# Kernel optimization log

Hardware: AMD Instinct MI355X
Metric: run time of the kernel (lower is better)

## Reference

```python
import jax, jax.numpy as jnp
import numpy as np

B, T, C, HS = 4, 4096, 1024, 64


def setup_inputs() -> dict:
    key = jax.random.key(0)
    kx, kq, kk, kv = jax.random.split(key, 4)
    x = jax.random.normal(kx, (B, T, C), dtype=jnp.float32)
    s = 1.0 / np.sqrt(C)
    Wq = jax.random.normal(kq, (C, HS), dtype=jnp.float32) * s
    Wk = jax.random.normal(kk, (C, HS), dtype=jnp.float32) * s
    Wv = jax.random.normal(kv, (C, HS), dtype=jnp.float32) * s
    return {"x": x, "Wq": Wq, "Wk": Wk, "Wv": Wv}


def reference(x, Wq, Wk, Wv):
    # q,k,v: [B, T, HS]
    q = x @ Wq
    k = x @ Wk
    v = x @ Wv
    scale = k.shape[-1] ** -0.5
    # full T x T causal attention scores, as the torch module materializes
    scores = jnp.einsum('bqh,bkh->bqk', q, k) * scale  # [B, T, T]
    t = x.shape[1]
    causal = jnp.tril(jnp.ones((t, t), dtype=bool))
    scores = jnp.where(causal[None, :, :], scores, -jnp.inf)
    wei = jax.nn.softmax(scores, axis=-1)  # dropout = 0.0 (eval)
    out = jnp.einsum('bqk,bkh->bqh', wei, v)  # [B, T, HS]
    return out
```

## Files before the change

### kernel.cpp

```cpp
#include <hip/hip_runtime.h>
#include <math.h>

#define BB 4
#define TT 4096
#define CC 1024
#define HS 64
#define MM (BB*TT)

typedef __attribute__((ext_vector_type(8))) short short8;
typedef __attribute__((ext_vector_type(4))) float f32x4;
typedef __attribute__((ext_vector_type(4))) unsigned short ushort4v;

__device__ __forceinline__ unsigned short f2bf(float f) {
    union { float f; unsigned u; } v; v.f = f;
    return (unsigned short)((v.u + 0x7fffu + ((v.u >> 16) & 1u)) >> 16);
}

__global__ __launch_bounds__(256) void prep_kernel(
    const float* __restrict__ Wq, const float* __restrict__ Wk,
    const float* __restrict__ Wv, unsigned short* __restrict__ Wt)
{
    const int which = blockIdx.x >> 4;
    const int k0 = (blockIdx.x & 15) * 64;
    const float* __restrict__ W = (which == 0) ? Wq : (which == 1) ? Wk : Wv;
    const float scale = (which == 0) ? 0.125f : 1.0f;
    __shared__ unsigned short lds[64][65];
    const int t = threadIdx.x;
    #pragma unroll
    for (int i = 0; i < 16; i++) {
        int idx = t + 256 * i;
        int r = idx >> 6, n = idx & 63;
        lds[r][n] = f2bf(W[(size_t)(k0 + r) * 64 + n] * scale);
    }
    __syncthreads();
    #pragma unroll
    for (int i = 0; i < 16; i++) {
        int idx = t + 256 * i;
        int n = idx >> 6, r = idx & 63;
        Wt[(which << 16) + (n << 10) + k0 + r] = lds[r][n];
    }
}

__global__ __launch_bounds__(256, 2) void qkv_mfma(
    const float* __restrict__ x, const unsigned short* __restrict__ Wt,
    unsigned short* __restrict__ qb, unsigned short* __restrict__ kb,
    unsigned short* __restrict__ vT)
{
    const int rt = blockIdx.x;
    __shared__ unsigned short xs[32][136];
    __shared__ unsigned short ws[192][136];

    const int t = threadIdx.x;
    const int w = t >> 6;
    const int lane = t & 63;
    const int quad = lane >> 4;
    const int c = lane & 15;

    float4 xreg[4];
    short8 wreg[12];
    #pragma unroll
    for (int i = 0; i < 4; i++) {
        int idx = t + 256 * i;
        int r = idx >> 5, c4 = (idx & 31) * 4;
        xreg[i] = *(const float4*)(x + (size_t)(rt * 32 + r) * CC + c4);
    }
    #pragma unroll
    for (int i = 0; i < 12; i++) {
        int idx = t + 256 * i;
        int n = idx >> 4, c8 = (idx & 15) * 8;
        wreg[i] = *(const short8*)(Wt + (size_t)n * CC + c8);
    }

    f32x4 acc[2][3];
    #pragma unroll
    for (int mt = 0; mt < 2; mt++)
        #pragma unroll
        for (int j = 0; j < 3; j++) acc[mt][j] = (f32x4){0.f, 0.f, 0.f, 0.f};

    for (int k0 = 0; k0 < CC; k0 += 128) {
        __syncthreads();
        #pragma unroll
        for (int i = 0; i < 4; i++) {
            int idx = t + 256 * i;
            int r = idx >> 5, c4 = (idx & 31) * 4;
            ushort4v p = { f2bf(xreg[i].x), f2bf(xreg[i].y), f2bf(xreg[i].z), f2bf(xreg[i].w) };
            *(ushort4v*)&xs[r][c4] = p;
        }
        #pragma unroll
        for (int i = 0; i < 12; i++) {
            int idx = t + 256 * i;
            int n = idx >> 4, c8 = (idx & 15) * 8;
            *(short8*)&ws[n][c8] = wreg[i];
        }
        if (k0 + 128 < CC) {
            #pragma unroll
            for (int i = 0; i < 4; i++) {
                int idx = t + 256 * i;
                int r = idx >> 5, c4 = (idx & 31) * 4;
                xreg[i] = *(const float4*)(x + (size_t)(rt * 32 + r) * CC + k0 + 128 + c4);
            }
            #pragma unroll
            for (int i = 0; i < 12; i++) {
                int idx = t + 256 * i;
                int n = idx >> 4, c8 = (idx & 15) * 8;
                wreg[i] = *(const short8*)(Wt + (size_t)n * CC + k0 + 128 + c8);
            }
        }
        __syncthreads();
        #pragma unroll
        for (int ks = 0; ks < 4; ks++) {
            short8 af[2], bf[3];
            #pragma unroll
            for (int mt = 0; mt < 2; mt++)
                af[mt] = *(const short8*)&xs[16 * mt + c][ks * 32 + quad * 8];
            #pragma unroll
            for (int j = 0; j < 3; j++)
                bf[j] = *(const short8*)&ws[16 * (w + 4 * j) + c][ks * 32 + quad * 8];
            #pragma unroll
            for (int mt = 0; mt < 2; mt++)
                #pragma unroll
                for (int j = 0; j < 3; j++)
                    acc[mt][j] = __builtin_amdgcn_mfma_f32_16x16x32_bf16(af[mt], bf[j], acc[mt][j], 0, 0, 0);
        }
    }

    __syncthreads();
    unsigned short (*vtb)[72] = (unsigned short (*)[72])ws;
    #pragma unroll
    for (int mt = 0; mt < 2; mt++) {
        int grow = rt * 32 + 16 * mt + quad * 4;
        #pragma unroll
        for (int reg = 0; reg < 4; reg++) {
            qb[(size_t)(grow + reg) * HS + 16 * w + c] = f2bf(acc[mt][0][reg]);
            kb[(size_t)(grow + reg) * HS + 16 * w + c] = f2bf(acc[mt][1][reg]);
            vtb[16 * w + c][16 * mt + quad * 4 + reg] = f2bf(acc[mt][2][reg]);
        }
    }
    __syncthreads();
    {
        const int b  = rt >> 7;
        const int t0 = (rt & 127) * 32;
        int d = t >> 2, c8 = (t & 3) * 8;
        short8 v0 = *(const short8*)&vtb[d][c8];
        *(short8*)(vT + (size_t)b * HS * TT + (size_t)d * TT + t0 + c8) = v0;
    }
}

__global__ __launch_bounds__(256, 4) void attn_mfma(
    const unsigned short* __restrict__ qb, const unsigned short* __restrict__ kb,
    const unsigned short* __restrict__ vT, float* __restrict__ Opart,
    float* __restrict__ lpart)
{
    const int bid = blockIdx.x;
    const int qt = (TT / 64 - 1) - (bid >> 4);
    const int j  = (bid >> 2) & 3;
    const int b  = bid & 3;

    __shared__ unsigned short ks[64][72];
    __shared__ unsigned short vt[64][72];
    __shared__ unsigned short ps[4][16][72];

    const int t = threadIdx.x;
    const int w = t >> 6;
    const int lane = t & 63;
    const int quad = lane >> 4;
    const int c = lane & 15;
    const int qrow = qt * 64 + 16 * w;

    short8 aq[2];
    #pragma unroll
    for (int kstep = 0; kstep < 2; kstep++)
        aq[kstep] = *(const short8*)(qb + (size_t)(b * TT + qrow + c) * HS + kstep * 32 + quad * 8);

    const int nkt = (qt >= j) ? ((qt - j) >> 2) + 1 : 0;
    const unsigned short* Kb = kb + (size_t)b * TT * HS;
    const unsigned short* Vb = vT + (size_t)b * HS * TT;

    const int srow = t >> 3;
    const int sc8  = (t & 7) * 8;

    short8 kreg[2], vreg[2];
    if (nkt > 0) {
        const int kt0 = j * 64;
        #pragma unroll
        for (int i = 0; i < 2; i++) {
            kreg[i] = *(const short8*)(Kb + (size_t)(kt0 + srow + 32 * i) * HS + sc8);
            vreg[i] = *(const short8*)(Vb + (size_t)(srow + 32 * i) * TT + kt0 + sc8);
        }
    }

    float l[4] = {0.f, 0.f, 0.f, 0.f};
    f32x4 oacc[4];
    #pragma unroll
    for (int dt = 0; dt < 4; dt++) oacc[dt] = (f32x4){0.f, 0.f, 0.f, 0.f};

    for (int i = 0; i < nkt; i++) {
        const int kt = j + 4 * i;
        const int kt0 = kt * 64;
        __syncthreads();
        #pragma unroll
        for (int ii = 0; ii < 2; ii++) {
            *(short8*)&ks[srow + 32 * ii][sc8] = kreg[ii];
            *(short8*)&vt[srow + 32 * ii][sc8] = vreg[ii];
        }
        if (i + 1 < nkt) {
            const int nb = kt0 + 256;
            #pragma unroll
            for (int ii = 0; ii < 2; ii++) {
                kreg[ii] = *(const short8*)(Kb + (size_t)(nb + srow + 32 * ii) * HS + sc8);
                vreg[ii] = *(const short8*)(Vb + (size_t)(srow + 32 * ii) * TT + nb + sc8);
            }
        }
        __syncthreads();

        f32x4 sc[4];
        #pragma unroll
        for (int st = 0; st < 4; st++) sc[st] = (f32x4){0.f, 0.f, 0.f, 0.f};
        #pragma unroll
        for (int kstep = 0; kstep < 2; kstep++) {
            #pragma unroll
            for (int st = 0; st < 4; st++) {
                short8 bf = *(const short8*)&ks[16 * st + c][kstep * 32 + quad * 8];
                sc[st] = __builtin_amdgcn_mfma_f32_16x16x32_bf16(aq[kstep], bf, sc[st], 0, 0, 0);
            }
        }
        if (kt == qt) {
            #pragma unroll
            for (int st = 0; st < 4; st++)
                #pragma unroll
                for (int reg = 0; reg < 4; reg++) {
                    int kg = kt0 + 16 * st + c;
                    int qg = qrow + quad * 4 + reg;
                    float p = (kg <= qg) ? __expf(sc[st][reg]) : 0.f;
                    sc[st][reg] = p;
                    l[reg] += p;
                }
        } else {
            #pragma unroll
            for (int st = 0; st < 4; st++)
                #pragma unroll
                for (int reg = 0; reg < 4; reg++) {
                    float p = __expf(sc[st][reg]);
                    sc[st][reg] = p;
                    l[reg] += p;
                }
        }
        #pragma unroll
        for (int st = 0; st < 4; st++)
            #pragma unroll
            for (int reg = 0; reg < 4; reg++)
                ps[w][quad * 4 + reg][16 * st + c] = f2bf(sc[st][reg]);

        #pragma unroll
        for (int kstep = 0; kstep < 2; kstep++) {
            short8 ap = *(const short8*)&ps[w][c][kstep * 32 + quad * 8];
            #pragma unroll
            for (int dt = 0; dt < 4; dt++) {
                short8 bv = *(const short8*)&vt[16 * dt + c][kstep * 32 + quad * 8];
                oacc[dt] = __builtin_amdgcn_mfma_f32_16x16x32_bf16(ap, bv, oacc[dt], 0, 0, 0);
            }
        }
    }

    #pragma unroll
    for (int reg = 0; reg < 4; reg++)
        #pragma unroll
        for (int msk = 1; msk < 16; msk <<= 1)
            l[reg] += __shfl_xor(l[reg], msk);

    float* __restrict__ Oj = Opart + (size_t)j * MM * HS;
    #pragma unroll
    for (int dt = 0; dt < 4; dt++)
        #pragma unroll
        for (int reg = 0; reg < 4; reg++)
            Oj[(size_t)(b * TT + qrow + quad * 4 + reg) * HS + 16 * dt + c] = oacc[dt][reg];
    if (c == 0)
        #pragma unroll
        for (int reg = 0; reg < 4; reg++)
            lpart[(size_t)j * MM + b * TT + qrow + quad * 4 + reg] = l[reg];
}

__global__ __launch_bounds__(256) void combine_kernel(
    const float* __restrict__ Opart, const float* __restrict__ lpart,
    float* __restrict__ out)
{
    const int id = blockIdx.x * 256 + threadIdx.x;
    const int row = id >> 4;
    float l = lpart[row] + lpart[MM + row] + lpart[2 * MM + row] + lpart[3 * MM + row];
    const float4* O = (const float4*)Opart;
    const size_t stride = (size_t)MM * HS / 4;
    float4 a = O[id], b = O[id + stride], c = O[id + 2 * stride], d = O[id + 3 * stride];
    float inv = 1.f / l;
    float4 r;
    r.x = (a.x + b.x + c.x + d.x) * inv;
    r.y = (a.y + b.y + c.y + d.y) * inv;
    r.z = (a.z + b.z + c.z + d.z) * inv;
    r.w = (a.w + b.w + c.w + d.w) * inv;
    ((float4*)out)[id] = r;
}

extern "C" void kernel_launch(void* const* d_in, const int* in_sizes, int n_in,
                              void* d_out, int out_size, void* d_ws, size_t ws_size,
                              hipStream_t stream) {
    const float* x  = (const float*)d_in[0];
    const float* Wq = (const float*)d_in[1];
    const float* Wk = (const float*)d_in[2];
    const float* Wv = (const float*)d_in[3];
    float* out = (float*)d_out;

    unsigned short* Wt   = (unsigned short*)d_ws;
    unsigned short* qbuf = Wt + 3 * 64 * 1024;
    unsigned short* kbuf = qbuf + (size_t)MM * HS;
    unsigned short* vTb  = kbuf + (size_t)MM * HS;
    float* Opart = (float*)(vTb + (size_t)MM * HS);
    float* lpart = Opart + 4 * (size_t)MM * HS;

    prep_kernel<<<48, 256, 0, stream>>>(Wq, Wk, Wv, Wt);
    qkv_mfma<<<MM / 32, 256, 0, stream>>>(x, Wt, qbuf, kbuf, vTb);
    attn_mfma<<<BB * (TT / 64) * 4, 256, 0, stream>>>(qbuf, kbuf, vTb, Opart, lpart);
    combine_kernel<<<1024, 256, 0, stream>>>(Opart, lpart, out);
}
```

Baseline: 136.8 us.

## Use 128-row query tiles with 8-way KV split and packed bf16 conversion

```diff
diff --git a/kernel.cpp b/kernel.cpp
--- a/kernel.cpp
+++ b/kernel.cpp
@@ -6,6 +6,7 @@
 #define CC 1024
 #define HS 64
 #define MM (BB*TT)
+#define KSPLIT 8
 
 typedef __attribute__((ext_vector_type(8))) short short8;
 typedef __attribute__((ext_vector_type(4))) float f32x4;
@@ -14,6 +15,12 @@
 __device__ __forceinline__ unsigned short f2bf(float f) {
     union { float f; unsigned u; } v; v.f = f;
     return (unsigned short)((v.u + 0x7fffu + ((v.u >> 16) & 1u)) >> 16);
+}
+
+__device__ __forceinline__ unsigned cvt_pk_bf16(float lo, float hi) {
+    unsigned r;
+    asm("v_cvt_pk_bf16_f32 %0, %1, %2" : "=v"(r) : "v"(lo), "v"(hi));
+    return r;
 }
 
 __global__ __launch_bounds__(256) void prep_kernel(
@@ -152,27 +159,30 @@
     float* __restrict__ lpart)
 {
     const int bid = blockIdx.x;
-    const int qt = (TT / 64 - 1) - (bid >> 4);
-    const int j  = (bid >> 2) & 3;
+    const int qt = (TT / 128 - 1) - (bid >> 5);
+    const int j  = (bid >> 2) & 7;
     const int b  = bid & 3;
 
     __shared__ unsigned short ks[64][72];
     __shared__ unsigned short vt[64][72];
-    __shared__ unsigned short ps[4][16][72];
+    __shared__ unsigned short ps[4][32][72];
 
     const int t = threadIdx.x;
     const int w = t >> 6;
     const int lane = t & 63;
     const int quad = lane >> 4;
     const int c = lane & 15;
-    const int qrow = qt * 64 + 16 * w;
-
-    short8 aq[2];
-    #pragma unroll
-    for (int kstep = 0; kstep < 2; kstep++)
-        aq[kstep] = *(const short8*)(qb + (size_t)(b * TT + qrow + c) * HS + kstep * 32 + quad * 8);
-
-    const int nkt = (qt >= j) ? ((qt - j) >> 2) + 1 : 0;
+    const int qrow = qt * 128 + 32 * w;
+
+    short8 aq[2][2];
+    #pragma unroll
+    for (int mt = 0; mt < 2; mt++)
+        #pragma unroll
+        for (int kstep = 0; kstep < 2; kstep++)
+            aq[mt][kstep] = *(const short8*)(qb + (size_t)(b * TT + qrow + 16 * mt + c) * HS + kstep * 32 + quad * 8);
+
+    const int lastkt = 2 * qt + 1;
+    const int nkt = (lastkt >= j) ? ((lastkt - j) >> 3) + 1 : 0;
     const unsigned short* Kb = kb + (size_t)b * TT * HS;
     const unsigned short* Vb = vT + (size_t)b * HS * TT;
 
@@ -189,13 +199,45 @@
         }
     }
 
-    float l[4] = {0.f, 0.f, 0.f, 0.f};
-    f32x4 oacc[4];
-    #pragma unroll
-    for (int dt = 0; dt < 4; dt++) oacc[dt] = (f32x4){0.f, 0.f, 0.f, 0.f};
+    float l[2][4] = {{0.f,0.f,0.f,0.f},{0.f,0.f,0.f,0.f}};
+    f32x4 oacc[2][4];
+    #pragma unroll
+    for (int mt = 0; mt < 2; mt++)
+        #pragma unroll
+        for (int dt = 0; dt < 4; dt++) oacc[mt][dt] = (f32x4){0.f, 0.f, 0.f, 0.f};
+
+#define SCORE_ST(MASKC) do { \
+    _Pragma("unroll") \
+    for (int st = 0; st < 4; st++) { \
+        f32x4 s[2]; \
+        s[0] = (f32x4){0.f,0.f,0.f,0.f}; s[1] = (f32x4){0.f,0.f,0.f,0.f}; \
+        _Pragma("unroll") \
+        for (int kstep = 0; kstep < 2; kstep++) { \
+            short8 bf = *(const short8*)&ks[16 * st + c][kstep * 32 + quad * 8]; \
+            s[0] = __builtin_amdgcn_mfma_f32_16x16x32_bf16(aq[0][kstep], bf, s[0], 0, 0, 0); \
+            s[1] = __builtin_amdgcn_mfma_f32_16x16x32_bf16(aq[1][kstep], bf, s[1], 0, 0, 0); \
+        } \
+        _Pragma("unroll") \
+        for (int mt = 0; mt < 2; mt++) { \
+            _Pragma("unroll") \
+            for (int reg = 0; reg < 4; reg++) { \
+                int kg = kt0 + 16 * st + c; (void)kg; \
+                int qg = qrow + 16 * mt + quad * 4 + reg; (void)qg; \
+                float p = (MASKC) ? __expf(s[mt][reg]) : 0.f; \
+                s[mt][reg] = p; \
+                l[mt][reg] += p; \
+            } \
+            unsigned p01 = cvt_pk_bf16(s[mt][0], s[mt][1]); \
+            unsigned p23 = cvt_pk_bf16(s[mt][2], s[mt][3]); \
+            ps[w][16 * mt + quad * 4 + 0][16 * st + c] = (unsigned short)p01; \
+            ps[w][16 * mt + quad * 4 + 1][16 * st + c] = (unsigned short)(p01 >> 16); \
+            ps[w][16 * mt + quad * 4 + 2][16 * st + c] = (unsigned short)p23; \
+            ps[w][16 * mt + quad * 4 + 3][16 * st + c] = (unsigned short)(p23 >> 16); \
+        } \
+    } } while (0)
 
     for (int i = 0; i < nkt; i++) {
-        const int kt = j + 4 * i;
+        const int kt = j + KSPLIT * i;
         const int kt0 = kt * 64;
         __syncthreads();
         #pragma unroll
@@ -203,81 +245,63 @@
             *(short8*)&ks[srow + 32 * ii][sc8] = kreg[ii];
             *(short8*)&vt[srow + 32 * ii][sc8] = vreg[ii];
         }
+        __syncthreads();
+
         if (i + 1 < nkt) {
-            const int nb = kt0 + 256;
+            const int nb = kt0 + KSPLIT * 64;
             #pragma unroll
             for (int ii = 0; ii < 2; ii++) {
                 kreg[ii] = *(const short8*)(Kb + (size_t)(nb + srow + 32 * ii) * HS + sc8);
                 vreg[ii] = *(const short8*)(Vb + (size_t)(srow + 32 * ii) * TT + nb + sc8);
             }
         }
-        __syncthreads();
-
-        f32x4 sc[4];
-        #pragma unroll
-        for (int st = 0; st < 4; st++) sc[st] = (f32x4){0.f, 0.f, 0.f, 0.f};
+
+        if (kt0 > qrow + 31) continue;
+
+        if (kt >= 2 * qt) {
+            SCORE_ST(kg <= qg);
+        } else {
+            SCORE_ST(1);
+        }
+
         #pragma unroll
         for (int kstep = 0; kstep < 2; kstep++) {
-            #pragma unroll
-            for (int st = 0; st < 4; st++) {
-                short8 bf = *(const short8*)&ks[16 * st + c][kstep * 32 + quad * 8];
-                sc[st] = __builtin_amdgcn_mfma_f32_16x16x32_bf16(aq[kstep], bf, sc[st], 0, 0, 0);
-            }
-        }
-        if (kt == qt) {
-            #pragma unroll
-            for (int st = 0; st < 4; st++)
-                #pragma unroll
-                for (int reg = 0; reg < 4; reg++) {
-                    int kg = kt0 + 16 * st + c;
-                    int qg = qrow + quad * 4 + reg;
-                    float p = (kg <= qg) ? __expf(sc[st][reg]) : 0.f;
-                    sc[st][reg] = p;
-                    l[reg] += p;
-                }
-        } else {
-            #pragma unroll
-            for (int st = 0; st < 4; st++)
-                #pragma unroll
-                for (int reg = 0; reg < 4; reg++) {
-                    float p = __expf(sc[st][reg]);
-                    sc[st][reg] = p;
-                    l[reg] += p;
-                }
-        }
-        #pragma unroll
-        for (int st = 0; st < 4; st++)
-            #pragma unroll
-            for (int reg = 0; reg < 4; reg++)
-                ps[w][quad * 4 + reg][16 * st + c] = f2bf(sc[st][reg]);
-
-        #pragma unroll
-        for (int kstep = 0; kstep < 2; kstep++) {
-            short8 ap = *(const short8*)&ps[w][c][kstep * 32 + quad * 8];
+            short8 ap[2];
+            #pragma unroll
+            for (int mt = 0; mt < 2; mt++)
+                ap[mt] = *(const short8*)&ps[w][16 * mt + c][kstep * 32 + quad * 8];
             #pragma unroll
             for (int dt = 0; dt < 4; dt++) {
                 short8 bv = *(const short8*)&vt[16 * dt + c][kstep * 32 + quad * 8];
-                oacc[dt] = __builtin_amdgcn_mfma_f32_16x16x32_bf16(ap, bv, oacc[dt], 0, 0, 0);
+                oacc[0][dt] = __builtin_amdgcn_mfma_f32_16x16x32_bf16(ap[0], bv, oacc[0][dt], 0, 0, 0);
+                oacc[1][dt] = __builtin_amdgcn_mfma_f32_16x16x32_bf16(ap[1], bv, oacc[1][dt], 0, 0, 0);
             }
         }
     }
-
-    #pragma unroll
-    for (int reg = 0; reg < 4; reg++)
-        #pragma unroll
-        for (int msk = 1; msk < 16; msk <<= 1)
-            l[reg] += __shfl_xor(l[reg], msk);
+#undef SCORE_ST
+
+    #pragma unroll
+    for (int mt = 0; mt < 2; mt++)
+        #pragma unroll
+        for (int reg = 0; reg < 4; reg++)
+            #pragma unroll
+            for (int msk = 1; msk < 16; msk <<= 1)
+                l[mt][reg] += __shfl_xor(l[mt][reg], msk);
 
     float* __restrict__ Oj = Opart + (size_t)j * MM * HS;
     #pragma unroll
-    for (int dt = 0; dt < 4; dt++)
-        #pragma unroll
-        for (int reg = 0; reg < 4; reg++)
-            Oj[(size_t)(b * TT + qrow + quad * 4 + reg) * HS + 16 * dt + c] = oacc[dt][reg];
+    for (int mt = 0; mt < 2; mt++)
+        #pragma unroll
+        for (int dt = 0; dt < 4; dt++)
+            #pragma unroll
+            for (int reg = 0; reg < 4; reg++)
+                Oj[(size_t)(b * TT + qrow + 16 * mt + quad * 4 + reg) * HS + 16 * dt + c] = oacc[mt][dt][reg];
     if (c == 0)
         #pragma unroll
-        for (int reg = 0; reg < 4; reg++)
-            lpart[(size_t)j * MM + b * TT + qrow + quad * 4 + reg] = l[reg];
+        for (int mt = 0; mt < 2; mt++)
+            #pragma unroll
+            for (int reg = 0; reg < 4; reg++)
+                lpart[(size_t)j * MM + b * TT + qrow + 16 * mt + quad * 4 + reg] = l[mt][reg];
 }
 
 __global__ __launch_bounds__(256) void combine_kernel(
@@ -286,16 +310,19 @@
 {
     const int id = blockIdx.x * 256 + threadIdx.x;
     const int row = id >> 4;
-    float l = lpart[row] + lpart[MM + row] + lpart[2 * MM + row] + lpart[3 * MM + row];
+    float l = 0.f;
+    #pragma unroll
+    for (int j = 0; j < KSPLIT; j++) l += lpart[(size_t)j * MM + row];
     const float4* O = (const float4*)Opart;
     const size_t stride = (size_t)MM * HS / 4;
-    float4 a = O[id], b = O[id + stride], c = O[id + 2 * stride], d = O[id + 3 * stride];
+    float4 r = {0.f, 0.f, 0.f, 0.f};
+    #pragma unroll
+    for (int j = 0; j < KSPLIT; j++) {
+        float4 a = O[id + (size_t)j * stride];
+        r.x += a.x; r.y += a.y; r.z += a.z; r.w += a.w;
+    }
     float inv = 1.f / l;
-    float4 r;
-    r.x = (a.x + b.x + c.x + d.x) * inv;
-    r.y = (a.y + b.y + c.y + d.y) * inv;
-    r.z = (a.z + b.z + c.z + d.z) * inv;
-    r.w = (a.w + b.w + c.w + d.w) * inv;
+    r.x *= inv; r.y *= inv; r.z *= inv; r.w *= inv;
     ((float4*)out)[id] = r;
 }
 
@@ -313,10 +340,10 @@
     unsigned short* kbuf = qbuf + (size_t)MM * HS;
     unsigned short* vTb  = kbuf + (size_t)MM * HS;
     float* Opart = (float*)(vTb + (size_t)MM * HS);
-    float* lpart = Opart + 4 * (size_t)MM * HS;
+    float* lpart = Opart + (size_t)KSPLIT * MM * HS;
 
     prep_kernel<<<48, 256, 0, stream>>>(Wq, Wk, Wv, Wt);
     qkv_mfma<<<MM / 32, 256, 0, stream>>>(x, Wt, qbuf, kbuf, vTb);
-    attn_mfma<<<BB * (TT / 64) * 4, 256, 0, stream>>>(qbuf, kbuf, vTb, Opart, lpart);
+    attn_mfma<<<BB * (TT / 128) * KSPLIT, 256, 0, stream>>>(qbuf, kbuf, vTb, Opart, lpart);
     combine_kernel<<<1024, 256, 0, stream>>>(Opart, lpart, out);
 }
```

Measured after the change: 137.4 us. Within noise of the previous version (+0.5%).
